# Optimization experiments

Measured on AMD Instinct MI355X. Metric: run time of the kernel, lower is better.

## Reference

```python
import jax, jax.numpy as jnp
import numpy as np

B, S, D_IN, D_H = 8, 2048, 512, 512

def setup_inputs() -> dict:
    key = jax.random.key(0)
    ks = jax.random.split(key, 7)
    scale = 1.0 / np.sqrt(D_IN)
    return {
        "x": jax.random.normal(ks[0], (B, S, D_IN), dtype=jnp.float32),
        "Wq": jax.random.uniform(ks[1], (D_IN, D_H), jnp.float32, -scale, scale),
        "bq": jax.random.uniform(ks[2], (D_H,), jnp.float32, -scale, scale),
        "Wk": jax.random.uniform(ks[3], (D_IN, D_H), jnp.float32, -scale, scale),
        "bk": jax.random.uniform(ks[4], (D_H,), jnp.float32, -scale, scale),
        "Wv": jax.random.uniform(ks[5], (D_IN, D_H), jnp.float32, -scale, scale),
        "bv": jax.random.uniform(ks[6], (D_H,), jnp.float32, -scale, scale),
    }

def reference(x, Wq, bq, Wk, bk, Wv, bv):
    q = jnp.einsum("bsd,dh->bsh", x, Wq) + bq  # [B,S,H]
    k = jnp.einsum("bsd,dh->bsh", x, Wk) + bk
    v = jnp.einsum("bsd,dh->bsh", x, Wv) + bv
    # NOTE: original has NO 1/sqrt(d) scaling — faithful reproduction
    scores = jnp.einsum("bqh,bkh->bqk", q, k)  # [B,S,S]
    probs = jax.nn.softmax(scores, axis=-1)
    return jnp.einsum("bqk,bkh->bqh", probs, v)
```

## Files before the change

### kernel.cpp

```cpp
#include <hip/hip_runtime.h>


typedef __attribute__((ext_vector_type(8))) _Float16 f16x8;
typedef __attribute__((ext_vector_type(8))) short bf16x8;
typedef __attribute__((ext_vector_type(4))) float f32x4;

__device__ __forceinline__ unsigned short f2h(float f) {
  _Float16 h = (_Float16)f;
  return *(unsigned short*)&h;
}
__device__ __forceinline__ unsigned short f2bf(float f) {
  unsigned int u = __float_as_uint(f);
  unsigned int r = (u + 0x7fffu + ((u >> 16) & 1u)) >> 16;
  return (unsigned short)r;
}
__device__ __forceinline__ float bf2f(unsigned short h) {
  return __uint_as_float(((unsigned int)h) << 16);
}

__device__ __forceinline__ void load_lds16(const void* g, void* l) {
  __builtin_amdgcn_global_load_lds(
      (const __attribute__((address_space(1))) unsigned int*)g,
      (__attribute__((address_space(3))) unsigned int*)l, 16, 0, 0);
}

__global__ __launch_bounds__(256) void convx_kernel(const float* __restrict__ x,
                                                    unsigned short* __restrict__ xh) {
  int i = blockIdx.x * 256 + threadIdx.x;
  float4 v = ((const float4*)x)[i];
  union { unsigned short h[4]; short4 s4; } u;
  u.h[0] = f2h(v.x); u.h[1] = f2h(v.y); u.h[2] = f2h(v.z); u.h[3] = f2h(v.w);
  ((short4*)xh)[i] = u.s4;
}

__global__ __launch_bounds__(256) void convw_kernel(
    const float* __restrict__ W0, const float* __restrict__ W1,
    const float* __restrict__ W2, unsigned short* __restrict__ Wt) {
  const float* W = (blockIdx.z == 0) ? W0 : (blockIdx.z == 1) ? W1 : W2;
  unsigned short* t = Wt + (size_t)blockIdx.z * 512 * 512;
  __shared__ float tile[32][33];
  int tx = threadIdx.x, ty = threadIdx.y;
  int h0 = blockIdx.x * 32, d0 = blockIdx.y * 32;
  for (int i = ty; i < 32; i += 8) tile[i][tx] = W[(long)(d0 + i) * 512 + h0 + tx];
  __syncthreads();
  for (int i = ty; i < 32; i += 8)
    t[(long)(h0 + i) * 512 + d0 + tx] = f2h(tile[tx][i]);
}

__global__ __launch_bounds__(256) void gemm_qkv_kernel(
    const unsigned short* __restrict__ A,
    const unsigned short* __restrict__ Bt,
    unsigned short* __restrict__ Qo, unsigned short* __restrict__ Ko,
    unsigned short* __restrict__ VTo,
    const float* __restrict__ bq, const float* __restrict__ bk,
    const float* __restrict__ bv) {
  __shared__ alignas(16) unsigned short As[2][4096];
  __shared__ alignas(16) unsigned short Bs[2][4096];
  const int t = threadIdx.x;
  const long long bm = (long long)blockIdx.x * 128;
  const long long bn = (long long)blockIdx.y * 128;

  const int ar = t >> 2;
  const int ac = (t & 3) * 8;

  f32x4 acc[4][4];
#pragma unroll
  for (int i = 0; i < 4; i++)
#pragma unroll
    for (int j = 0; j < 4; j++) acc[i][j] = {0.f, 0.f, 0.f, 0.f};

  const int lane = t & 63;
  const int wave = t >> 6;
  const int wm = (wave & 1) * 64;
  const int wn = (wave >> 1) * 64;
  const int fm = lane & 15;
  const int k8 = (lane >> 4) * 8;

#pragma unroll
  for (int r = 0; r < 2; r++)
    load_lds16(A + (bm + r * 64 + ar) * 512 + ac, &As[0][r * 2048 + t * 8]);
#pragma unroll
  for (int r = 0; r < 2; r++)
    load_lds16(Bt + (bn + r * 64 + ar) * 512 + ac, &Bs[0][r * 2048 + t * 8]);

  for (int ktt = 0; ktt < 16; ++ktt) {
    const int cur = ktt & 1;
    const int nxt = cur ^ 1;
    if (ktt < 15) {
      const int kc = (ktt + 1) * 32;
#pragma unroll
      for (int r = 0; r < 2; r++)
        load_lds16(A + (bm + r * 64 + ar) * 512 + kc + ac, &As[nxt][r * 2048 + t * 8]);
#pragma unroll
      for (int r = 0; r < 2; r++)
        load_lds16(Bt + (bn + r * 64 + ar) * 512 + kc + ac, &Bs[nxt][r * 2048 + t * 8]);
      asm volatile("s_waitcnt vmcnt(4)" ::: "memory");
    } else {
      asm volatile("s_waitcnt vmcnt(0)" ::: "memory");
    }
    __builtin_amdgcn_s_barrier();
    __builtin_amdgcn_sched_barrier(0);

    f16x8 af[4], bfr[4];
#pragma unroll
    for (int i = 0; i < 4; i++)
      af[i] = *(const f16x8*)&As[cur][(wm + i * 16 + fm) * 32 + k8];
#pragma unroll
    for (int j = 0; j < 4; j++)
      bfr[j] = *(const f16x8*)&Bs[cur][(wn + j * 16 + fm) * 32 + k8];
    __builtin_amdgcn_s_setprio(1);
#pragma unroll
    for (int i = 0; i < 4; i++)
#pragma unroll
      for (int j = 0; j < 4; j++)
        acc[i][j] = __builtin_amdgcn_mfma_f32_16x16x32_f16(af[i], bfr[j], acc[i][j], 0, 0, 0);
    __builtin_amdgcn_s_setprio(0);
    asm volatile("s_waitcnt lgkmcnt(0)" ::: "memory");
    __builtin_amdgcn_s_barrier();
  }

  const int crow = (lane >> 4) * 4;
  const int ccol = lane & 15;
#pragma unroll
  for (int j = 0; j < 4; j++) {
    const long long col = bn + wn + j * 16 + ccol;
    float bias = (col < 512) ? bq[col] : (col < 1024) ? bk[col - 512] : bv[col - 1024];
#pragma unroll
    for (int i = 0; i < 4; i++) {
      const long long row0 = bm + wm + i * 16 + crow;
      if (col >= 1024) {
        const long long b = row0 >> 11;
        const long long s = row0 & 2047;
        const long long dcol = col - 1024;
        union { unsigned short h[4]; short4 s4; } u;
#pragma unroll
        for (int r = 0; r < 4; r++) u.h[r] = f2bf(acc[i][j][r] + bias);
        const long long unit = b * 64 + (s >> 5);
        const int L = ((int)dcol * 64 + (int)(s & 31) * 2) ^ ((((int)dcol >> 1) & 7) << 4);
        *(short4*)((char*)VTo + unit * 32768 + L) = u.s4;
      } else {
        unsigned short* dst = (col < 512) ? (Qo + row0 * 512 + col)
                                          : (Ko + row0 * 512 + (col - 512));
#pragma unroll
        for (int r = 0; r < 4; r++) dst[(size_t)r * 512] = f2h(acc[i][j][r] + bias);
      }
    }
  }
}

__global__ __launch_bounds__(512, 2) void attn_fused_kernel(
    const unsigned short* __restrict__ Qg,
    const unsigned short* __restrict__ Kg,
    const unsigned short* __restrict__ Vt,
    float* __restrict__ out) {
  __shared__ alignas(16) unsigned short SB[2][16384];
  __shared__ alignas(16) unsigned short Qh[16384];
  __shared__ alignas(16) unsigned short Ps[8192];
  __shared__ float rsw[4][64];

  const int t = threadIdx.x;
  const int lane = t & 63;
  const int w = t >> 6;
  const int fm = lane & 15;
  const int g = lane >> 4;
  const int qh = w & 1;
  const int kg = w >> 1;
  const int b = blockIdx.x & 7;
  const int q0 = (blockIdx.x >> 3) << 6;

  const unsigned short* Qb = Qg + ((size_t)b * 2048 + q0) * 512;
  const unsigned short* Kb = Kg + (size_t)b * 2048 * 512;
  const unsigned short* Vb = Vt + (size_t)b * 2048 * 512;

  int ksrc[4], qsrc[4]; unsigned int sdst[4];
#pragma unroll
  for (int r = 0; r < 4; ++r) {
    const int L = r * 8192 + t * 16;
    sdst[r] = L >> 1;
    const int kr = L >> 8;
    ksrc[r] = kr * 512 + (((L & 255) ^ ((kr & 7) << 4)) >> 1);
    const int qr = L >> 9;
    qsrc[r] = qr * 512 + (((L & 511) ^ ((qr & 7) << 4)) >> 1);
  }

#pragma unroll
  for (int r = 0; r < 4; ++r) load_lds16(Qb + qsrc[r], &SB[0][sdst[r]]);
#pragma unroll
  for (int r = 0; r < 4; ++r) load_lds16(Qb + 256 + qsrc[r], &Qh[sdst[r]]);
  asm volatile("s_waitcnt vmcnt(4)" ::: "memory");
  __builtin_amdgcn_s_barrier();

  const int swz = (fm & 7) << 4;
  const int vswz = ((fm >> 1) & 7) << 4;
  f16x8 qf[2][8];
#pragma unroll
  for (int j = 0; j < 2; ++j)
#pragma unroll
    for (int ds = 0; ds < 8; ++ds)
      qf[j][ds] = *(const f16x8*)((const char*)SB[0] +
          (qh * 32 + j * 16 + fm) * 512 + ((g * 16 + ds * 64) ^ swz));
  asm volatile("s_waitcnt lgkmcnt(0)" ::: "memory");
  __builtin_amdgcn_s_barrier();
#pragma unroll
  for (int r = 0; r < 4; ++r) load_lds16(Kb + ksrc[r], &SB[0][sdst[r]]);

  f32x4 oacc[2][8];
#pragma unroll
  for (int i = 0; i < 2; ++i)
#pragma unroll
    for (int jj = 0; jj < 8; ++jj) oacc[i][jj] = {0.f, 0.f, 0.f, 0.f};
  float psum0 = 0.f, psum1 = 0.f;
  f32x4 sacc[2][2];

  for (int kt = 0; kt < 16; ++kt) {
    const size_t kbase = (size_t)kt * 65536;
#pragma unroll
    for (int u = 0; u < 8; ++u) {
      unsigned short* cur = SB[u & 1];
      unsigned short* nxt = SB[(u & 1) ^ 1];
      if (u < 3) {
#pragma unroll
        for (int r = 0; r < 4; ++r)
          load_lds16(Kb + kbase + (u + 1) * 128 + ksrc[r], &nxt[sdst[r]]);
      } else if (u < 7) {
        const unsigned short* vs = Vb + (size_t)(kt * 4 + (u - 3)) * 16384;
#pragma unroll
        for (int r = 0; r < 4; ++r) load_lds16(vs + sdst[r], &nxt[sdst[r]]);
      } else if (kt < 15) {
#pragma unroll
        for (int r = 0; r < 4; ++r)
          load_lds16(Kb + kbase + 65536 + ksrc[r], &nxt[sdst[r]]);
      }
      if (kt == 15 && u == 7)
        asm volatile("s_waitcnt vmcnt(0)" ::: "memory");
      else
        asm volatile("s_waitcnt vmcnt(4)" ::: "memory");
      __builtin_amdgcn_s_barrier();
      __builtin_amdgcn_sched_barrier(0);

      __builtin_amdgcn_s_setprio(1);
      if (u < 4) {
        if (u == 0) {
          sacc[0][0] = {0.f, 0.f, 0.f, 0.f}; sacc[0][1] = {0.f, 0.f, 0.f, 0.f};
          sacc[1][0] = {0.f, 0.f, 0.f, 0.f}; sacc[1][1] = {0.f, 0.f, 0.f, 0.f};
        }
#pragma unroll
        for (int s = 0; s < 4; ++s) {
          const f16x8 a0 = *(const f16x8*)((const char*)cur +
              (kg * 32 + fm) * 256 + ((g * 16 + s * 64) ^ swz));
          const f16x8 a1 = *(const f16x8*)((const char*)cur +
              (kg * 32 + 16 + fm) * 256 + ((g * 16 + s * 64) ^ swz));
          f16x8 b0, b1;
          if (u < 2) {
            b0 = qf[0][u * 4 + s]; b1 = qf[1][u * 4 + s];
          } else {
            const int dz = (g * 16 + ((u - 2) * 4 + s) * 64) ^ swz;
            b0 = *(const f16x8*)((const char*)Qh + (qh * 32 + fm) * 512 + dz);
            b1 = *(const f16x8*)((const char*)Qh + (qh * 32 + 16 + fm) * 512 + dz);
          }
          sacc[0][0] = __builtin_amdgcn_mfma_f32_16x16x32_f16(a0, b0, sacc[0][0], 0, 0, 0);
          sacc[0][1] = __builtin_amdgcn_mfma_f32_16x16x32_f16(a0, b1, sacc[0][1], 0, 0, 0);
          sacc[1][0] = __builtin_amdgcn_mfma_f32_16x16x32_f16(a1, b0, sacc[1][0], 0, 0, 0);
          sacc[1][1] = __builtin_amdgcn_mfma_f32_16x16x32_f16(a1, b1, sacc[1][1], 0, 0, 0);
        }
        if (u == 3) {
#pragma unroll
          for (int i = 0; i < 2; ++i)
#pragma unroll
            for (int j = 0; j < 2; ++j) {
              const int q = qh * 32 + j * 16 + fm;
              const int k2 = (kg * 32 + i * 16 + g * 4) * 2;
              union { unsigned short h[4]; short4 s4; } uu;
              float s0 = 0.f;
#pragma unroll
              for (int r = 0; r < 4; ++r) {
                const unsigned short pb = f2bf(__expf(sacc[i][j][r]));
                uu.h[r] = pb; s0 += bf2f(pb);
              }
              if (j == 0) psum0 += s0; else psum1 += s0;
              *(short4*)((char*)Ps + q * 256 + (k2 ^ swz)) = uu.s4;
            }
        }
      } else {
        const int ju = u - 4;
        const bf16x8 p0 = *(const bf16x8*)((const char*)Ps +
            (qh * 32 + fm) * 256 + ((ju * 64 + g * 16) ^ swz));
        const bf16x8 p1 = *(const bf16x8*)((const char*)Ps +
            (qh * 32 + 16 + fm) * 256 + ((ju * 64 + g * 16) ^ swz));
#pragma unroll
        for (int jj = 0; jj < 8; ++jj) {
          const bf16x8 vf = *(const bf16x8*)((const char*)cur +
              ((((kg * 128 + jj * 16 + fm) * 64) + g * 16) ^ vswz));
          oacc[0][jj] = __builtin_amdgcn_mfma_f32_16x16x32_bf16(p0, vf, oacc[0][jj], 0, 0, 0);
          oacc[1][jj] = __builtin_amdgcn_mfma_f32_16x16x32_bf16(p1, vf, oacc[1][jj], 0, 0, 0);
        }
      }
      __builtin_amdgcn_s_setprio(0);
      asm volatile("s_waitcnt lgkmcnt(0)" ::: "memory");
      __builtin_amdgcn_s_barrier();
    }
  }

  psum0 += __shfl_xor(psum0, 16); psum0 += __shfl_xor(psum0, 32);
  psum1 += __shfl_xor(psum1, 16); psum1 += __shfl_xor(psum1, 32);
  if (g == 0) {
    rsw[kg][qh * 32 + fm] = psum0;
    rsw[kg][qh * 32 + 16 + fm] = psum1;
  }
  __syncthreads();

  float* ob = out + ((size_t)b * 2048 + q0) * 512;
#pragma unroll
  for (int i = 0; i < 2; ++i) {
    float inv[4];
#pragma unroll
    for (int r = 0; r < 4; ++r) {
      const int q = qh * 32 + i * 16 + g * 4 + r;
      inv[r] = 1.0f / (rsw[0][q] + rsw[1][q] + rsw[2][q] + rsw[3][q]);
    }
#pragma unroll
    for (int jj = 0; jj < 8; ++jj) {
      const int d = kg * 128 + jj * 16 + fm;
#pragma unroll
      for (int r = 0; r < 4; ++r)
        ob[(size_t)(qh * 32 + i * 16 + g * 4 + r) * 512 + d] = oacc[i][jj][r] * inv[r];
    }
  }
}

extern "C" void kernel_launch(void* const* d_in, const int* in_sizes, int n_in,
                              void* d_out, int out_size, void* d_ws, size_t ws_size,
                              hipStream_t stream) {
  const float* x  = (const float*)d_in[0];
  const float* Wq = (const float*)d_in[1];
  const float* bq = (const float*)d_in[2];
  const float* Wk = (const float*)d_in[3];
  const float* bk = (const float*)d_in[4];
  const float* Wv = (const float*)d_in[5];
  const float* bv = (const float*)d_in[6];
  float* out = (float*)d_out;

  const size_t SZ = (size_t)16384 * 512 * 2;
  char* p = (char*)d_ws;
  unsigned short* xh = (unsigned short*)p; p += SZ;
  unsigned short* Wt = (unsigned short*)p; p += (size_t)3 * 512 * 512 * 2;
  unsigned short* Qb = (unsigned short*)p; p += SZ;
  unsigned short* Kb = (unsigned short*)p; p += SZ;
  unsigned short* VT = (unsigned short*)p; p += SZ;

  convx_kernel<<<8192, 256, 0, stream>>>(x, xh);
  convw_kernel<<<dim3(16, 16, 3), dim3(32, 8), 0, stream>>>(Wq, Wk, Wv, Wt);
  gemm_qkv_kernel<<<dim3(128, 12), 256, 0, stream>>>(xh, Wt, Qb, Kb, VT, bq, bk, bv);
  attn_fused_kernel<<<256, 512, 0, stream>>>(Qb, Kb, VT, out);
}
```

Baseline: 233.8 us.

## Halve attention query tile to 32 rows and key tile to 64

The fused attention kernel now handles 32 query rows per block (512 blocks) and streams 64-key tiles, with half-size LDS buffers and register accumulators. Launch bounds are raised to 4 blocks per SM, and the V-transpose layout written by the QKV GEMM changes to match the smaller tiles. The aim is more parallelism and occupancy, since 256 blocks underfill the GPU's CUs. The cost is that K and V are reloaded twice as often per query and each barrier-separated step does fewer MFMAs, which raises sync overhead relative to compute.

```diff
diff --git a/kernel.cpp b/kernel.cpp
--- a/kernel.cpp
+++ b/kernel.cpp
@@ -135,9 +135,9 @@
         union { unsigned short h[4]; short4 s4; } u;
 #pragma unroll
         for (int r = 0; r < 4; r++) u.h[r] = f2bf(acc[i][j][r] + bias);
-        const long long unit = b * 64 + (s >> 5);
-        const int L = ((int)dcol * 64 + (int)(s & 31) * 2) ^ ((((int)dcol >> 1) & 7) << 4);
-        *(short4*)((char*)VTo + unit * 32768 + L) = u.s4;
+        const long long unit = b * 128 + (s >> 5) * 2 + (dcol >> 8);
+        const int L = (((int)dcol & 255) * 64 + (int)(s & 31) * 2) ^ ((((int)dcol >> 1) & 7) << 4);
+        *(short4*)((char*)VTo + unit * 16384 + L) = u.s4;
       } else {
         unsigned short* dst = (col < 512) ? (Qo + row0 * 512 + col)
                                           : (Ko + row0 * 512 + (col - 512));
@@ -148,15 +148,15 @@
   }
 }
 
-__global__ __launch_bounds__(512, 2) void attn_fused_kernel(
+__global__ __launch_bounds__(512, 4) void attn_fused_kernel(
     const unsigned short* __restrict__ Qg,
     const unsigned short* __restrict__ Kg,
     const unsigned short* __restrict__ Vt,
     float* __restrict__ out) {
-  __shared__ alignas(16) unsigned short SB[2][16384];
-  __shared__ alignas(16) unsigned short Qh[16384];
-  __shared__ alignas(16) unsigned short Ps[8192];
-  __shared__ float rsw[4][64];
+  __shared__ alignas(16) unsigned short SB[2][8192];
+  __shared__ alignas(16) unsigned short Qh[8192];
+  __shared__ alignas(16) unsigned short Ps[2048];
+  __shared__ float rsw[4][32];
 
   const int t = threadIdx.x;
   const int lane = t & 63;
@@ -166,15 +166,15 @@
   const int qh = w & 1;
   const int kg = w >> 1;
   const int b = blockIdx.x & 7;
-  const int q0 = (blockIdx.x >> 3) << 6;
+  const int q0 = (blockIdx.x >> 3) << 5;
 
   const unsigned short* Qb = Qg + ((size_t)b * 2048 + q0) * 512;
   const unsigned short* Kb = Kg + (size_t)b * 2048 * 512;
   const unsigned short* Vb = Vt + (size_t)b * 2048 * 512;
 
-  int ksrc[4], qsrc[4]; unsigned int sdst[4];
-#pragma unroll
-  for (int r = 0; r < 4; ++r) {
+  int ksrc[2], qsrc[2]; unsigned int sdst[2];
+#pragma unroll
+  for (int r = 0; r < 2; ++r) {
     const int L = r * 8192 + t * 16;
     sdst[r] = L >> 1;
     const int kr = L >> 8;
@@ -184,115 +184,95 @@
   }
 
 #pragma unroll
-  for (int r = 0; r < 4; ++r) load_lds16(Qb + qsrc[r], &SB[0][sdst[r]]);
-#pragma unroll
-  for (int r = 0; r < 4; ++r) load_lds16(Qb + 256 + qsrc[r], &Qh[sdst[r]]);
-  asm volatile("s_waitcnt vmcnt(4)" ::: "memory");
+  for (int r = 0; r < 2; ++r) load_lds16(Qb + qsrc[r], &SB[0][sdst[r]]);
+#pragma unroll
+  for (int r = 0; r < 2; ++r) load_lds16(Qb + 256 + qsrc[r], &Qh[sdst[r]]);
+  asm volatile("s_waitcnt vmcnt(2)" ::: "memory");
   __builtin_amdgcn_s_barrier();
 
   const int swz = (fm & 7) << 4;
   const int vswz = ((fm >> 1) & 7) << 4;
-  f16x8 qf[2][8];
-#pragma unroll
-  for (int j = 0; j < 2; ++j)
-#pragma unroll
-    for (int ds = 0; ds < 8; ++ds)
-      qf[j][ds] = *(const f16x8*)((const char*)SB[0] +
-          (qh * 32 + j * 16 + fm) * 512 + ((g * 16 + ds * 64) ^ swz));
+  f16x8 qf[8];
+#pragma unroll
+  for (int ds = 0; ds < 8; ++ds)
+    qf[ds] = *(const f16x8*)((const char*)SB[0] +
+        (qh * 16 + fm) * 512 + ((g * 16 + ds * 64) ^ swz));
   asm volatile("s_waitcnt lgkmcnt(0)" ::: "memory");
   __builtin_amdgcn_s_barrier();
 #pragma unroll
-  for (int r = 0; r < 4; ++r) load_lds16(Kb + ksrc[r], &SB[0][sdst[r]]);
-
-  f32x4 oacc[2][8];
-#pragma unroll
-  for (int i = 0; i < 2; ++i)
-#pragma unroll
-    for (int jj = 0; jj < 8; ++jj) oacc[i][jj] = {0.f, 0.f, 0.f, 0.f};
-  float psum0 = 0.f, psum1 = 0.f;
-  f32x4 sacc[2][2];
-
-  for (int kt = 0; kt < 16; ++kt) {
-    const size_t kbase = (size_t)kt * 65536;
+  for (int r = 0; r < 2; ++r) load_lds16(Kb + ksrc[r], &SB[0][sdst[r]]);
+
+  f32x4 oacc[8];
+#pragma unroll
+  for (int jj = 0; jj < 8; ++jj) oacc[jj] = {0.f, 0.f, 0.f, 0.f};
+  float psum0 = 0.f;
+  f32x4 sacc;
+
+  for (int kt = 0; kt < 32; ++kt) {
+    const size_t kbase = (size_t)kt * 32768;
 #pragma unroll
     for (int u = 0; u < 8; ++u) {
-      unsigned short* cur = SB[u & 1];
+      unsigned short* curb = SB[u & 1];
       unsigned short* nxt = SB[(u & 1) ^ 1];
       if (u < 3) {
 #pragma unroll
-        for (int r = 0; r < 4; ++r)
+        for (int r = 0; r < 2; ++r)
           load_lds16(Kb + kbase + (u + 1) * 128 + ksrc[r], &nxt[sdst[r]]);
       } else if (u < 7) {
-        const unsigned short* vs = Vb + (size_t)(kt * 4 + (u - 3)) * 16384;
-#pragma unroll
-        for (int r = 0; r < 4; ++r) load_lds16(vs + sdst[r], &nxt[sdst[r]]);
-      } else if (kt < 15) {
-#pragma unroll
-        for (int r = 0; r < 4; ++r)
-          load_lds16(Kb + kbase + 65536 + ksrc[r], &nxt[sdst[r]]);
+        const unsigned short* vs = Vb + (size_t)(kt * 4 + (u - 3)) * 8192;
+#pragma unroll
+        for (int r = 0; r < 2; ++r) load_lds16(vs + sdst[r], &nxt[sdst[r]]);
+      } else if (kt < 31) {
+#pragma unroll
+        for (int r = 0; r < 2; ++r)
+          load_lds16(Kb + kbase + 32768 + ksrc[r], &nxt[sdst[r]]);
       }
-      if (kt == 15 && u == 7)
+      if (kt == 31 && u == 7)
         asm volatile("s_waitcnt vmcnt(0)" ::: "memory");
       else
-        asm volatile("s_waitcnt vmcnt(4)" ::: "memory");
+        asm volatile("s_waitcnt vmcnt(2)" ::: "memory");
       __builtin_amdgcn_s_barrier();
       __builtin_amdgcn_sched_barrier(0);
 
       __builtin_amdgcn_s_setprio(1);
       if (u < 4) {
-        if (u == 0) {
-          sacc[0][0] = {0.f, 0.f, 0.f, 0.f}; sacc[0][1] = {0.f, 0.f, 0.f, 0.f};
-          sacc[1][0] = {0.f, 0.f, 0.f, 0.f}; sacc[1][1] = {0.f, 0.f, 0.f, 0.f};
-        }
+        if (u == 0) sacc = {0.f, 0.f, 0.f, 0.f};
 #pragma unroll
         for (int s = 0; s < 4; ++s) {
-          const f16x8 a0 = *(const f16x8*)((const char*)cur +
-              (kg * 32 + fm) * 256 + ((g * 16 + s * 64) ^ swz));
-          const f16x8 a1 = *(const f16x8*)((const char*)cur +
-              (kg * 32 + 16 + fm) * 256 + ((g * 16 + s * 64) ^ swz));
-          f16x8 b0, b1;
+          const f16x8 a0 = *(const f16x8*)((const char*)curb +
+              (kg * 16 + fm) * 256 + ((g * 16 + s * 64) ^ swz));
+          f16x8 b0;
           if (u < 2) {
-            b0 = qf[0][u * 4 + s]; b1 = qf[1][u * 4 + s];
+            b0 = qf[u * 4 + s];
           } else {
             const int dz = (g * 16 + ((u - 2) * 4 + s) * 64) ^ swz;
-            b0 = *(const f16x8*)((const char*)Qh + (qh * 32 + fm) * 512 + dz);
-            b1 = *(const f16x8*)((const char*)Qh + (qh * 32 + 16 + fm) * 512 + dz);
+            b0 = *(const f16x8*)((const char*)Qh + (qh * 16 + fm) * 512 + dz);
           }
-          sacc[0][0] = __builtin_amdgcn_mfma_f32_16x16x32_f16(a0, b0, sacc[0][0], 0, 0, 0);
-          sacc[0][1] = __builtin_amdgcn_mfma_f32_16x16x32_f16(a0, b1, sacc[0][1], 0, 0, 0);
-          sacc[1][0] = __builtin_amdgcn_mfma_f32_16x16x32_f16(a1, b0, sacc[1][0], 0, 0, 0);
-          sacc[1][1] = __builtin_amdgcn_mfma_f32_16x16x32_f16(a1, b1, sacc[1][1], 0, 0, 0);
+          sacc = __builtin_amdgcn_mfma_f32_16x16x32_f16(a0, b0, sacc, 0, 0, 0);
         }
         if (u == 3) {
-#pragma unroll
-          for (int i = 0; i < 2; ++i)
-#pragma unroll
-            for (int j = 0; j < 2; ++j) {
-              const int q = qh * 32 + j * 16 + fm;
-              const int k2 = (kg * 32 + i * 16 + g * 4) * 2;
-              union { unsigned short h[4]; short4 s4; } uu;
-              float s0 = 0.f;
-#pragma unroll
-              for (int r = 0; r < 4; ++r) {
-                const unsigned short pb = f2bf(__expf(sacc[i][j][r]));
-                uu.h[r] = pb; s0 += bf2f(pb);
-              }
-              if (j == 0) psum0 += s0; else psum1 += s0;
-              *(short4*)((char*)Ps + q * 256 + (k2 ^ swz)) = uu.s4;
-            }
+          const int q = qh * 16 + fm;
+          const int k2 = kg * 32 + g * 8;
+          union { unsigned short h[4]; short4 s4; } uu;
+          float sthis = 0.f;
+#pragma unroll
+          for (int r = 0; r < 4; ++r) {
+            const unsigned short pb = f2bf(__expf(sacc[r]));
+            uu.h[r] = pb; sthis += bf2f(pb);
+          }
+          psum0 += sthis;
+          *(short4*)((char*)Ps + q * 128 + (k2 ^ swz)) = uu.s4;
         }
       } else {
-        const int ju = u - 4;
+        const int kh = (u - 4) >> 1;
+        const int dh = (u - 4) & 1;
         const bf16x8 p0 = *(const bf16x8*)((const char*)Ps +
-            (qh * 32 + fm) * 256 + ((ju * 64 + g * 16) ^ swz));
-        const bf16x8 p1 = *(const bf16x8*)((const char*)Ps +
-            (qh * 32 + 16 + fm) * 256 + ((ju * 64 + g * 16) ^ swz));
-#pragma unroll
-        for (int jj = 0; jj < 8; ++jj) {
-          const bf16x8 vf = *(const bf16x8*)((const char*)cur +
-              ((((kg * 128 + jj * 16 + fm) * 64) + g * 16) ^ vswz));
-          oacc[0][jj] = __builtin_amdgcn_mfma_f32_16x16x32_bf16(p0, vf, oacc[0][jj], 0, 0, 0);
-          oacc[1][jj] = __builtin_amdgcn_mfma_f32_16x16x32_bf16(p1, vf, oacc[1][jj], 0, 0, 0);
+            (qh * 16 + fm) * 128 + ((kh * 64 + g * 16) ^ swz));
+#pragma unroll
+        for (int jj = 0; jj < 4; ++jj) {
+          const bf16x8 vf = *(const bf16x8*)((const char*)curb +
+              ((((kg * 64 + jj * 16 + fm) * 64) + g * 16) ^ vswz));
+          oacc[dh * 4 + jj] = __builtin_amdgcn_mfma_f32_16x16x32_bf16(p0, vf, oacc[dh * 4 + jj], 0, 0, 0);
         }
       }
       __builtin_amdgcn_s_setprio(0);
@@ -302,30 +282,25 @@
   }
 
   psum0 += __shfl_xor(psum0, 16); psum0 += __shfl_xor(psum0, 32);
-  psum1 += __shfl_xor(psum1, 16); psum1 += __shfl_xor(psum1, 32);
-  if (g == 0) {
-    rsw[kg][qh * 32 + fm] = psum0;
-    rsw[kg][qh * 32 + 16 + fm] = psum1;
-  }
+  if (g == 0) rsw[kg][qh * 16 + fm] = psum0;
   __syncthreads();
 
   float* ob = out + ((size_t)b * 2048 + q0) * 512;
-#pragma unroll
-  for (int i = 0; i < 2; ++i) {
-    float inv[4];
-#pragma unroll
-    for (int r = 0; r < 4; ++r) {
-      const int q = qh * 32 + i * 16 + g * 4 + r;
-      inv[r] = 1.0f / (rsw[0][q] + rsw[1][q] + rsw[2][q] + rsw[3][q]);
+  float inv[4];
+#pragma unroll
+  for (int r = 0; r < 4; ++r) {
+    const int q = qh * 16 + g * 4 + r;
+    inv[r] = 1.0f / (rsw[0][q] + rsw[1][q] + rsw[2][q] + rsw[3][q]);
+  }
+#pragma unroll
+  for (int dh = 0; dh < 2; ++dh)
+#pragma unroll
+    for (int jj = 0; jj < 4; ++jj) {
+      const int d = dh * 256 + kg * 64 + jj * 16 + fm;
+#pragma unroll
+      for (int r = 0; r < 4; ++r)
+        ob[(size_t)(qh * 16 + g * 4 + r) * 512 + d] = oacc[dh * 4 + jj][r] * inv[r];
     }
-#pragma unroll
-    for (int jj = 0; jj < 8; ++jj) {
-      const int d = kg * 128 + jj * 16 + fm;
-#pragma unroll
-      for (int r = 0; r < 4; ++r)
-        ob[(size_t)(qh * 32 + i * 16 + g * 4 + r) * 512 + d] = oacc[i][jj][r] * inv[r];
-    }
-  }
 }
 
 extern "C" void kernel_launch(void* const* d_in, const int* in_sizes, int n_in,
@@ -351,5 +326,5 @@
   convx_kernel<<<8192, 256, 0, stream>>>(x, xh);
   convw_kernel<<<dim3(16, 16, 3), dim3(32, 8), 0, stream>>>(Wq, Wk, Wv, Wt);
   gemm_qkv_kernel<<<dim3(128, 12), 256, 0, stream>>>(xh, Wt, Qb, Kb, VT, bq, bk, bv);
-  attn_fused_kernel<<<256, 512, 0, stream>>>(Qb, Kb, VT, out);
-}
+  attn_fused_kernel<<<512, 512, 0, stream>>>(Qb, Kb, VT, out);
+}
```

After: 252.0 us. 7.8% more time.
